# Optimization experiments

Hardware: AMD Instinct MI355X
Metric: run time of the kernel (lower is better)

The kernel has to match this reference:

```python
import jax, jax.numpy as jnp
import numpy as np

N_USER = 1_000_000
N_ITEM = 100_000
E = 16          # embedding_size
O = 16          # out_size per head
H = 4           # head_num
HID = 32        # hidden_size
B = 8192        # batch
S = 200         # sample_num
L = 50          # history length
NSUPP = 50_000  # supp_user_num


def _xavier(key, shape):
    fan_in, fan_out = shape[-2], shape[-1]
    std = np.sqrt(2.0 / (fan_in + fan_out))
    return (jax.random.normal(key, shape) * std).astype(jnp.float32)


def setup_inputs() -> dict:
    key = jax.random.key(0)
    ks = jax.random.split(key, 16)
    uid = jax.random.randint(ks[0], (B,), 0, N_USER)
    iid = jax.random.randint(ks[1], (B,), 0, N_ITEM)
    return {
        "user_embedding": _xavier(ks[2], (N_USER, E)),
        "item_embedding": _xavier(ks[3], (N_ITEM, E)),
        "wq": _xavier(ks[4], (H, E, O)),   # per-head Wq (no bias)
        "wk": _xavier(ks[5], (H, E, O)),
        "wv": _xavier(ks[6], (H, O, O)),
        "w_out": _xavier(ks[7], (H * O, O)),
        "l1_w": _xavier(ks[8], (3 * E, HID)),
        "l1_b": jnp.full((HID,), 0.1, jnp.float32),
        "l2_w": _xavier(ks[9], (HID, HID // 2)),
        "l2_b": jnp.full((HID // 2,), 0.1, jnp.float32),
        "l3_w": _xavier(ks[10], (HID // 2, 1)),
        "l3_b": jnp.full((1,), 0.1, jnp.float32),
        "user_bias": jnp.zeros((N_USER, 1), jnp.float32),
        "item_bias": jnp.zeros((N_ITEM, 1), jnp.float32),
        "x": jnp.stack([uid, iid], axis=1),                          # [B,2]
        "history": jax.random.randint(ks[11], (B, L), 0, N_ITEM),    # [B,L]
        "history_len": jax.random.randint(ks[12], (B,), 1, L + 1),   # [B] >=1
        "supp_users": jax.random.randint(ks[13], (NSUPP,), 0, N_USER),
        "sample_index": jax.random.randint(ks[14], (H, B, S), 0, NSUPP),
    }


def reference(user_embedding, item_embedding, wq, wk, wv, w_out,
              l1_w, l1_b, l2_w, l2_b, l3_w, l3_b, user_bias, item_bias,
              x, history, history_len, supp_users, sample_index):
    user_id = x[:, 0]
    item_id = x[:, 1]

    # user init embedding = mean-by-len of full (unmasked) history, as in source
    hist_emb = item_embedding[history]                                # [B,L,E]
    user_init = hist_emb.sum(axis=1) / history_len[:, None].astype(jnp.float32)  # [B,E]

    # per-head GAT over sampled support users (all heads vectorized)
    nb = user_embedding[supp_users[sample_index]]                     # [H,B,S,E]
    q = jnp.einsum('be,heo->hbo', user_init, wq)                      # [H,B,O]
    k = jnp.einsum('hbse,heo->hbso', nb, wk)                          # [H,B,S,O]
    attn = jax.nn.softmax(jnp.einsum('hbo,hbso->hbs', q, k), axis=-1)
    ctx = jnp.einsum('hbs,hbso->hbo', attn, k)                        # [H,B,O]
    gat = jnp.einsum('hbo,hop->hbp', ctx, wv)                         # [H,B,O]
    gat = jnp.transpose(gat, (1, 0, 2)).reshape(B, H * O)             # concat heads

    user_emb = gat @ w_out                                            # [B,O]
    item_emb = item_embedding[item_id]                                # [B,E]
    interaction = user_emb * item_emb
    ratings = interaction.sum(axis=1)

    h = jnp.concatenate([user_emb, item_emb, interaction], axis=1)    # [B,3E]
    x1 = jnp.tanh(h @ l1_w + l1_b)
    x2 = jnp.tanh(x1 @ l2_w + l2_b)
    x3 = (x2 @ l3_w + l3_b).reshape(-1)

    ub = user_bias[user_id, 0]
    ib = item_bias[item_id, 0]
    return (ratings + x3) / 2.0 + ub + ib
```

## Files before the change

kernel.cpp:

```cpp
#include <hip/hip_runtime.h>
#include <math.h>

#define N_USERS 1000000
#define N_ITEMS 100000
#define EMB 16
#define OUTD 16
#define NH 4
#define HID 32
#define BB 8192
#define SS 200
#define LL 50
#define NSUPP 50000

typedef float v4f __attribute__((ext_vector_type(4)));
typedef _Float16 h4 __attribute__((ext_vector_type(4)));
typedef _Float16 h2 __attribute__((ext_vector_type(2)));

__global__ __launch_bounds__(256) void prep_kernel(
    const float* __restrict__ user_emb,
    const int*   __restrict__ supp_users,
    const float* __restrict__ wk,
    _Float16*    __restrict__ Ksupp,
    const float* __restrict__ item_emb,
    const int*   __restrict__ history,
    const int*   __restrict__ history_len,
    const float* __restrict__ wq,
    float*       __restrict__ qbuf)
{
    __shared__ float s_wk[NH * EMB * OUTD];
    __shared__ float s_u[16][EMB];
    __shared__ float s_ui[4][EMB];
    __shared__ float s_wq[NH * EMB * OUTD];

    int t = threadIdx.x;
    if (blockIdx.x < NSUPP / 16) {
        for (int i = t; i < NH * EMB * OUTD; i += 256) s_wk[i] = wk[i];
        int n0 = blockIdx.x * 16;
        {
            int ul = t >> 4, e = t & 15;
            int row = supp_users[n0 + ul];
            s_u[ul][e] = user_emb[(size_t)row * EMB + e];
        }
        __syncthreads();
        int h   = t >> 6;
        int sub = (t >> 4) & 3;
        int o   = t & 15;
#pragma unroll
        for (int r = 0; r < 4; ++r) {
            int ul = sub + 4 * r;
            float acc = 0.f;
#pragma unroll
            for (int e = 0; e < EMB; ++e)
                acc += s_u[ul][e] * s_wk[(h * EMB + e) * OUTD + o];
            Ksupp[((size_t)h * NSUPP + n0 + ul) * OUTD + o] = (_Float16)acc;
        }
    } else {
        for (int i = t; i < NH * EMB * OUTD; i += 256) s_wq[i] = wq[i];
        int g    = t >> 6;
        int lane = t & 63;
        int l4   = lane >> 4;
        int e    = lane & 15;
        int b    = (blockIdx.x - NSUPP / 16) * 4 + g;

        float sum = 0.f;
        for (int l = l4; l < LL; l += 4) {
            int it = __builtin_nontemporal_load(history + (size_t)b * LL + l);
            sum += item_emb[(size_t)it * EMB + e];
        }
        sum += __shfl_xor(sum, 16);
        sum += __shfl_xor(sum, 32);
        if (lane < EMB) s_ui[g][lane] = sum / (float)history_len[b];
        __syncthreads();

        int h = (t >> 4) & 3;
        int o = t & 15;
        float acc = 0.f;
#pragma unroll
        for (int ee = 0; ee < EMB; ++ee)
            acc += s_ui[g][ee] * s_wq[(h * EMB + ee) * OUTD + o];
        qbuf[((size_t)b * NH + h) * OUTD + o] = acc;
    }
}

__global__ __launch_bounds__(256, 8) void attn_kernel(
    const _Float16* __restrict__ Ksupp,
    const float* __restrict__ qbuf,
    const int*   __restrict__ sample_index,
    const float* __restrict__ wv,
    float*       __restrict__ gat)
{
    int blk   = blockIdx.x;
    int h     = (blk & 7) >> 1;
    int btile = ((blk >> 3) << 1) | (blk & 1);
    int wave  = threadIdx.x >> 6;
    int lane  = threadIdx.x & 63;
    int b     = btile * 4 + wave;
    int g     = lane >> 2;
    int qt    = lane & 3;

    const int* si = sample_index + ((size_t)h * BB + b) * SS;
    int pre0 = __builtin_nontemporal_load(si + lane);
    int pre1 = __builtin_nontemporal_load(si + lane + 64);
    int pre2 = __builtin_nontemporal_load(si + lane + 128);
    int pre3 = (lane < 8) ? __builtin_nontemporal_load(si + lane + 192) : 0;

    v4f qv = __builtin_nontemporal_load(
        (const v4f*)(qbuf + ((size_t)b * NH + h) * OUTD) + qt);
    h4 qh = __builtin_convertvector(qv, h4);
    h2 qlo = {qh.x, qh.y};
    h2 qhi = {qh.z, qh.w};

    const h4* K4 = (const h4*)(Ksupp + (size_t)h * NSUPP * OUTD);

    int idx[13];
#pragma unroll
    for (int r = 0; r < 13; ++r) {
        int pre = (r < 4) ? pre0 : (r < 8) ? pre1 : (r < 12) ? pre2 : pre3;
        idx[r] = __shfl(pre, (r & 3) * 16 + g, 64);
    }

    h4 kq[13];
#pragma unroll
    for (int r = 0; r < 13; ++r)
        kq[r] = K4[idx[r] * 4 + qt];

    float l = 0.f;
    v4f c = {0.f, 0.f, 0.f, 0.f};
#pragma unroll
    for (int r = 0; r < 13; ++r) {
        h2 klo = {kq[r].x, kq[r].y};
        h2 khi = {kq[r].z, kq[r].w};
        float p = __builtin_amdgcn_fdot2(klo, qlo,
                  __builtin_amdgcn_fdot2(khi, qhi, 0.f, false), false);
        p += __shfl_xor(p, 1);
        p += __shfl_xor(p, 2);
        float w = __expf(p);
        if (r == 12) w = (g < 8) ? w : 0.f;
        l += w;
        v4f kf = __builtin_convertvector(kq[r], v4f);
        c += w * kf;
    }
#pragma unroll
    for (int off = 4; off < 64; off <<= 1) {
        l   += __shfl_xor(l, off);
        c.x += __shfl_xor(c.x, off);
        c.y += __shfl_xor(c.y, off);
        c.z += __shfl_xor(c.z, off);
        c.w += __shfl_xor(c.w, off);
    }
    float inv = 1.f / l;

    float part = c.x * wv[((size_t)h * OUTD + qt * 4 + 0) * OUTD + g]
               + c.y * wv[((size_t)h * OUTD + qt * 4 + 1) * OUTD + g]
               + c.z * wv[((size_t)h * OUTD + qt * 4 + 2) * OUTD + g]
               + c.w * wv[((size_t)h * OUTD + qt * 4 + 3) * OUTD + g];
    part += __shfl_xor(part, 1);
    part += __shfl_xor(part, 2);
    if (qt == 0)
        gat[(size_t)b * (NH * OUTD) + h * OUTD + g] = part * inv;
}

__global__ __launch_bounds__(256) void epilogue_kernel(
    const float* __restrict__ gat,
    const float* __restrict__ item_emb,
    const float* __restrict__ w_out,
    const float* __restrict__ l1_w, const float* __restrict__ l1_b,
    const float* __restrict__ l2_w, const float* __restrict__ l2_b,
    const float* __restrict__ l3_w, const float* __restrict__ l3_b,
    const float* __restrict__ user_bias, const float* __restrict__ item_bias,
    const int*   __restrict__ x,
    float*       __restrict__ out)
{
    int t    = threadIdx.x;
    int g    = t >> 6;
    int lane = t & 63;
    int b    = blockIdx.x * 4 + g;

    __shared__ float s_gat[4][NH * OUTD];
    __shared__ float s_ue[4][OUTD];
    __shared__ float s_ie[4][EMB];
    __shared__ float s_x1[4][HID];
    __shared__ float s_x2[4][HID / 2];

    int uid = x[(size_t)b * 2 + 0];
    int iid = x[(size_t)b * 2 + 1];

    s_gat[g][lane] = gat[(size_t)b * (NH * OUTD) + lane];
    if (lane < EMB) s_ie[g][lane] = item_emb[(size_t)iid * EMB + lane];
    __syncthreads();

    if (lane < OUTD) {
        float acc = 0.f;
#pragma unroll
        for (int j = 0; j < NH * OUTD; ++j) acc += s_gat[g][j] * w_out[j * OUTD + lane];
        s_ue[g][lane] = acc;
    }
    __syncthreads();

    if (lane < HID) {
        float acc = l1_b[lane];
#pragma unroll
        for (int i = 0; i < EMB; ++i) {
            float ue = s_ue[g][i], ie = s_ie[g][i];
            acc += ue * l1_w[i * HID + lane]
                 + ie * l1_w[(EMB + i) * HID + lane]
                 + ue * ie * l1_w[(2 * EMB + i) * HID + lane];
        }
        s_x1[g][lane] = tanhf(acc);
    }
    __syncthreads();

    if (lane < HID / 2) {
        float acc = l2_b[lane];
#pragma unroll
        for (int j = 0; j < HID; ++j) acc += s_x1[g][j] * l2_w[j * (HID / 2) + lane];
        s_x2[g][lane] = tanhf(acc);
    }
    __syncthreads();

    if (lane == 0) {
        float x3 = l3_b[0];
#pragma unroll
        for (int j = 0; j < HID / 2; ++j) x3 += s_x2[g][j] * l3_w[j];
        float ratings = 0.f;
#pragma unroll
        for (int o = 0; o < OUTD; ++o) ratings += s_ue[g][o] * s_ie[g][o];
        out[b] = 0.5f * (ratings + x3) + user_bias[uid] + item_bias[iid];
    }
}

extern "C" void kernel_launch(void* const* d_in, const int* in_sizes, int n_in,
                              void* d_out, int out_size, void* d_ws, size_t ws_size,
                              hipStream_t stream) {
    const float* user_embedding = (const float*)d_in[0];
    const float* item_embedding = (const float*)d_in[1];
    const float* wq             = (const float*)d_in[2];
    const float* wk             = (const float*)d_in[3];
    const float* wv             = (const float*)d_in[4];
    const float* w_out          = (const float*)d_in[5];
    const float* l1_w           = (const float*)d_in[6];
    const float* l1_b           = (const float*)d_in[7];
    const float* l2_w           = (const float*)d_in[8];
    const float* l2_b           = (const float*)d_in[9];
    const float* l3_w           = (const float*)d_in[10];
    const float* l3_b           = (const float*)d_in[11];
    const float* user_bias      = (const float*)d_in[12];
    const float* item_bias      = (const float*)d_in[13];
    const int*   x              = (const int*)d_in[14];
    const int*   history        = (const int*)d_in[15];
    const int*   history_len    = (const int*)d_in[16];
    const int*   supp_users     = (const int*)d_in[17];
    const int*   sample_index   = (const int*)d_in[18];
    float* out = (float*)d_out;

    char* ws = (char*)d_ws;
    _Float16* Ksupp = (_Float16*)ws;
    ws += (size_t)NH * NSUPP * OUTD * sizeof(_Float16);
    float* qbuf  = (float*)ws;
    ws += (size_t)BB * NH * OUTD * sizeof(float);
    float* gat   = (float*)ws;

    prep_kernel<<<NSUPP / 16 + BB / 4, 256, 0, stream>>>(
        user_embedding, supp_users, wk, Ksupp,
        item_embedding, history, history_len, wq, qbuf);
    attn_kernel<<<NH * BB / 4, 256, 0, stream>>>(Ksupp, qbuf, sample_index, wv, gat);
    epilogue_kernel<<<BB / 4, 256, 0, stream>>>(
        gat, item_embedding, w_out, l1_w, l1_b, l2_w, l2_b, l3_w, l3_b,
        user_bias, item_bias, x, out);
}
```

Baseline: 220.1 us.

## Fold Wk into query and Wv, gather raw fp16 support embeddings, fuse epilogue

Reassociates the attention maths. The query is pre-multiplied by Wk^T, so scores come straight from raw support-user embeddings. Wk·Wv is precomputed so the context projection uses a single combined matrix. The per-head K table (4x50000x16) becomes one shared fp16 embedding table of 50000x16, which cuts table build work and the footprint of the gathers. The attention and epilogue kernels are merged, each block handling 4 batch rows across 4 head-waves, which removes the gat round-trip and one launch but lowers the launch bound to 4 and serializes 4 rows per wave.

Result: faster. 201.2 us (median of 2 runs) (-8.6%).

```diff
diff --git a/kernel.cpp b/kernel.cpp
--- a/kernel.cpp
+++ b/kernel.cpp
@@ -13,49 +13,42 @@
 #define NSUPP 50000
 
 typedef float v4f __attribute__((ext_vector_type(4)));
+typedef _Float16 h2 __attribute__((ext_vector_type(2)));
 typedef _Float16 h4 __attribute__((ext_vector_type(4)));
-typedef _Float16 h2 __attribute__((ext_vector_type(2)));
+
+#define WAVE_SYNC() do { asm volatile("s_waitcnt lgkmcnt(0)" ::: "memory"); \
+                         __builtin_amdgcn_sched_barrier(0); } while (0)
 
 __global__ __launch_bounds__(256) void prep_kernel(
     const float* __restrict__ user_emb,
     const int*   __restrict__ supp_users,
     const float* __restrict__ wk,
-    _Float16*    __restrict__ Ksupp,
+    const float* __restrict__ wq,
+    const float* __restrict__ wv,
     const float* __restrict__ item_emb,
     const int*   __restrict__ history,
     const int*   __restrict__ history_len,
-    const float* __restrict__ wq,
-    float*       __restrict__ qbuf)
+    _Float16*    __restrict__ tbl,
+    _Float16*    __restrict__ qtbuf,
+    float*       __restrict__ Wkv)
 {
-    __shared__ float s_wk[NH * EMB * OUTD];
-    __shared__ float s_u[16][EMB];
     __shared__ float s_ui[4][EMB];
     __shared__ float s_wq[NH * EMB * OUTD];
+    __shared__ float s_wk[NH * EMB * OUTD];
+    __shared__ float s_q[4][NH * OUTD];
 
     int t = threadIdx.x;
     if (blockIdx.x < NSUPP / 16) {
-        for (int i = t; i < NH * EMB * OUTD; i += 256) s_wk[i] = wk[i];
         int n0 = blockIdx.x * 16;
-        {
-            int ul = t >> 4, e = t & 15;
-            int row = supp_users[n0 + ul];
-            s_u[ul][e] = user_emb[(size_t)row * EMB + e];
-        }
-        __syncthreads();
-        int h   = t >> 6;
-        int sub = (t >> 4) & 3;
-        int o   = t & 15;
-#pragma unroll
-        for (int r = 0; r < 4; ++r) {
-            int ul = sub + 4 * r;
-            float acc = 0.f;
-#pragma unroll
-            for (int e = 0; e < EMB; ++e)
-                acc += s_u[ul][e] * s_wk[(h * EMB + e) * OUTD + o];
-            Ksupp[((size_t)h * NSUPP + n0 + ul) * OUTD + o] = (_Float16)acc;
-        }
-    } else {
-        for (int i = t; i < NH * EMB * OUTD; i += 256) s_wq[i] = wq[i];
+        int ul = t >> 4, e = t & 15;
+        int row = supp_users[n0 + ul];
+        tbl[(size_t)(n0 + ul) * EMB + e] =
+            (_Float16)user_emb[(size_t)row * EMB + e];
+    } else if (blockIdx.x < NSUPP / 16 + BB / 4) {
+        for (int i = t; i < NH * EMB * OUTD; i += 256) {
+            s_wq[i] = wq[i];
+            s_wk[i] = wk[i];
+        }
         int g    = t >> 6;
         int lane = t & 63;
         int l4   = lane >> 4;
@@ -78,90 +71,31 @@
 #pragma unroll
         for (int ee = 0; ee < EMB; ++ee)
             acc += s_ui[g][ee] * s_wq[(h * EMB + ee) * OUTD + o];
-        qbuf[((size_t)b * NH + h) * OUTD + o] = acc;
+        s_q[g][h * OUTD + o] = acc;
+        __syncthreads();
+
+        float qt = 0.f;
+#pragma unroll
+        for (int oo = 0; oo < OUTD; ++oo)
+            qt += s_wk[(h * EMB + o) * OUTD + oo] * s_q[g][h * OUTD + oo];
+        qtbuf[((size_t)b * NH + h) * EMB + o] = (_Float16)qt;
+    } else {
+        for (int i = t; i < NH * EMB * OUTD; i += 256) {
+            int h = i >> 8, e = (i >> 4) & 15, p = i & 15;
+            float a = 0.f;
+#pragma unroll
+            for (int o = 0; o < OUTD; ++o)
+                a += wk[(h * EMB + e) * OUTD + o] * wv[(h * OUTD + o) * OUTD + p];
+            Wkv[i] = a;
+        }
     }
 }
 
-__global__ __launch_bounds__(256, 8) void attn_kernel(
-    const _Float16* __restrict__ Ksupp,
-    const float* __restrict__ qbuf,
+__global__ __launch_bounds__(256, 4) void attn_epi_kernel(
+    const _Float16* __restrict__ tbl,
+    const _Float16* __restrict__ qtbuf,
     const int*   __restrict__ sample_index,
-    const float* __restrict__ wv,
-    float*       __restrict__ gat)
-{
-    int blk   = blockIdx.x;
-    int h     = (blk & 7) >> 1;
-    int btile = ((blk >> 3) << 1) | (blk & 1);
-    int wave  = threadIdx.x >> 6;
-    int lane  = threadIdx.x & 63;
-    int b     = btile * 4 + wave;
-    int g     = lane >> 2;
-    int qt    = lane & 3;
-
-    const int* si = sample_index + ((size_t)h * BB + b) * SS;
-    int pre0 = __builtin_nontemporal_load(si + lane);
-    int pre1 = __builtin_nontemporal_load(si + lane + 64);
-    int pre2 = __builtin_nontemporal_load(si + lane + 128);
-    int pre3 = (lane < 8) ? __builtin_nontemporal_load(si + lane + 192) : 0;
-
-    v4f qv = __builtin_nontemporal_load(
-        (const v4f*)(qbuf + ((size_t)b * NH + h) * OUTD) + qt);
-    h4 qh = __builtin_convertvector(qv, h4);
-    h2 qlo = {qh.x, qh.y};
-    h2 qhi = {qh.z, qh.w};
-
-    const h4* K4 = (const h4*)(Ksupp + (size_t)h * NSUPP * OUTD);
-
-    int idx[13];
-#pragma unroll
-    for (int r = 0; r < 13; ++r) {
-        int pre = (r < 4) ? pre0 : (r < 8) ? pre1 : (r < 12) ? pre2 : pre3;
-        idx[r] = __shfl(pre, (r & 3) * 16 + g, 64);
-    }
-
-    h4 kq[13];
-#pragma unroll
-    for (int r = 0; r < 13; ++r)
-        kq[r] = K4[idx[r] * 4 + qt];
-
-    float l = 0.f;
-    v4f c = {0.f, 0.f, 0.f, 0.f};
-#pragma unroll
-    for (int r = 0; r < 13; ++r) {
-        h2 klo = {kq[r].x, kq[r].y};
-        h2 khi = {kq[r].z, kq[r].w};
-        float p = __builtin_amdgcn_fdot2(klo, qlo,
-                  __builtin_amdgcn_fdot2(khi, qhi, 0.f, false), false);
-        p += __shfl_xor(p, 1);
-        p += __shfl_xor(p, 2);
-        float w = __expf(p);
-        if (r == 12) w = (g < 8) ? w : 0.f;
-        l += w;
-        v4f kf = __builtin_convertvector(kq[r], v4f);
-        c += w * kf;
-    }
-#pragma unroll
-    for (int off = 4; off < 64; off <<= 1) {
-        l   += __shfl_xor(l, off);
-        c.x += __shfl_xor(c.x, off);
-        c.y += __shfl_xor(c.y, off);
-        c.z += __shfl_xor(c.z, off);
-        c.w += __shfl_xor(c.w, off);
-    }
-    float inv = 1.f / l;
-
-    float part = c.x * wv[((size_t)h * OUTD + qt * 4 + 0) * OUTD + g]
-               + c.y * wv[((size_t)h * OUTD + qt * 4 + 1) * OUTD + g]
-               + c.z * wv[((size_t)h * OUTD + qt * 4 + 2) * OUTD + g]
-               + c.w * wv[((size_t)h * OUTD + qt * 4 + 3) * OUTD + g];
-    part += __shfl_xor(part, 1);
-    part += __shfl_xor(part, 2);
-    if (qt == 0)
-        gat[(size_t)b * (NH * OUTD) + h * OUTD + g] = part * inv;
-}
-
-__global__ __launch_bounds__(256) void epilogue_kernel(
-    const float* __restrict__ gat,
+    const float* __restrict__ Wkv,
     const float* __restrict__ item_emb,
     const float* __restrict__ w_out,
     const float* __restrict__ l1_w, const float* __restrict__ l1_b,
@@ -171,60 +105,123 @@
     const int*   __restrict__ x,
     float*       __restrict__ out)
 {
-    int t    = threadIdx.x;
-    int g    = t >> 6;
-    int lane = t & 63;
-    int b    = blockIdx.x * 4 + g;
-
     __shared__ float s_gat[4][NH * OUTD];
     __shared__ float s_ue[4][OUTD];
     __shared__ float s_ie[4][EMB];
     __shared__ float s_x1[4][HID];
     __shared__ float s_x2[4][HID / 2];
 
+    int h    = threadIdx.x >> 6;
+    int lane = threadIdx.x & 63;
+    int g    = lane >> 2;
+    int qt   = lane & 3;
+
+    const h4* U4 = (const h4*)tbl;
+
+    for (int bl = 0; bl < 4; ++bl) {
+        int b = blockIdx.x * 4 + bl;
+
+        const int* si = sample_index + ((size_t)h * BB + b) * SS;
+        int pre0 = __builtin_nontemporal_load(si + lane);
+        int pre1 = __builtin_nontemporal_load(si + lane + 64);
+        int pre2 = __builtin_nontemporal_load(si + lane + 128);
+        int pre3 = (lane < 8) ? __builtin_nontemporal_load(si + lane + 192) : 0;
+
+        h4 qh = ((const h4*)(qtbuf + ((size_t)b * NH + h) * EMB))[qt];
+        h2 qlo = {qh.x, qh.y};
+        h2 qhi = {qh.z, qh.w};
+
+        int idx[13];
+#pragma unroll
+        for (int r = 0; r < 13; ++r) {
+            int pre = (r < 4) ? pre0 : (r < 8) ? pre1 : (r < 12) ? pre2 : pre3;
+            idx[r] = __shfl(pre, (r & 3) * 16 + g, 64);
+        }
+
+        h4 kq[13];
+#pragma unroll
+        for (int r = 0; r < 13; ++r)
+            kq[r] = U4[(size_t)idx[r] * 4 + qt];
+
+        float l = 0.f;
+        v4f c = {0.f, 0.f, 0.f, 0.f};
+#pragma unroll
+        for (int r = 0; r < 13; ++r) {
+            h2 klo = {kq[r].x, kq[r].y};
+            h2 khi = {kq[r].z, kq[r].w};
+            float p = __builtin_amdgcn_fdot2(klo, qlo,
+                      __builtin_amdgcn_fdot2(khi, qhi, 0.f, false), false);
+            p += __shfl_xor(p, 1);
+            p += __shfl_xor(p, 2);
+            float w = __expf(p);
+            if (r == 12) w = (g < 8) ? w : 0.f;
+            l += w;
+            c += w * __builtin_convertvector(kq[r], v4f);
+        }
+#pragma unroll
+        for (int off = 4; off < 64; off <<= 1) {
+            l   += __shfl_xor(l, off);
+            c.x += __shfl_xor(c.x, off);
+            c.y += __shfl_xor(c.y, off);
+            c.z += __shfl_xor(c.z, off);
+            c.w += __shfl_xor(c.w, off);
+        }
+        float inv = 1.f / l;
+
+        float part = c.x * Wkv[((size_t)h * EMB + qt * 4 + 0) * OUTD + g]
+                   + c.y * Wkv[((size_t)h * EMB + qt * 4 + 1) * OUTD + g]
+                   + c.z * Wkv[((size_t)h * EMB + qt * 4 + 2) * OUTD + g]
+                   + c.w * Wkv[((size_t)h * EMB + qt * 4 + 3) * OUTD + g];
+        part += __shfl_xor(part, 1);
+        part += __shfl_xor(part, 2);
+        if (qt == 0)
+            s_gat[bl][h * OUTD + g] = part * inv;
+    }
+    __syncthreads();
+
+    int b   = blockIdx.x * 4 + h;
     int uid = x[(size_t)b * 2 + 0];
     int iid = x[(size_t)b * 2 + 1];
 
-    s_gat[g][lane] = gat[(size_t)b * (NH * OUTD) + lane];
-    if (lane < EMB) s_ie[g][lane] = item_emb[(size_t)iid * EMB + lane];
-    __syncthreads();
-
+    if (lane < EMB) s_ie[h][lane] = item_emb[(size_t)iid * EMB + lane];
     if (lane < OUTD) {
         float acc = 0.f;
 #pragma unroll
-        for (int j = 0; j < NH * OUTD; ++j) acc += s_gat[g][j] * w_out[j * OUTD + lane];
-        s_ue[g][lane] = acc;
-    }
-    __syncthreads();
+        for (int j = 0; j < NH * OUTD; ++j)
+            acc += s_gat[h][j] * w_out[j * OUTD + lane];
+        s_ue[h][lane] = acc;
+    }
+    WAVE_SYNC();
 
     if (lane < HID) {
         float acc = l1_b[lane];
 #pragma unroll
         for (int i = 0; i < EMB; ++i) {
-            float ue = s_ue[g][i], ie = s_ie[g][i];
+            float ue = s_ue[h][i], ie = s_ie[h][i];
             acc += ue * l1_w[i * HID + lane]
                  + ie * l1_w[(EMB + i) * HID + lane]
                  + ue * ie * l1_w[(2 * EMB + i) * HID + lane];
         }
-        s_x1[g][lane] = tanhf(acc);
-    }
-    __syncthreads();
+        s_x1[h][lane] = tanhf(acc);
+    }
+    WAVE_SYNC();
 
     if (lane < HID / 2) {
         float acc = l2_b[lane];
 #pragma unroll
-        for (int j = 0; j < HID; ++j) acc += s_x1[g][j] * l2_w[j * (HID / 2) + lane];
-        s_x2[g][lane] = tanhf(acc);
-    }
-    __syncthreads();
+        for (int j = 0; j < HID; ++j)
+            acc += s_x1[h][j] * l2_w[j * (HID / 2) + lane];
+        s_x2[h][lane] = tanhf(acc);
+    }
+    WAVE_SYNC();
 
     if (lane == 0) {
         float x3 = l3_b[0];
 #pragma unroll
-        for (int j = 0; j < HID / 2; ++j) x3 += s_x2[g][j] * l3_w[j];
+        for (int j = 0; j < HID / 2; ++j) x3 += s_x2[h][j] * l3_w[j];
         float ratings = 0.f;
 #pragma unroll
-        for (int o = 0; o < OUTD; ++o) ratings += s_ue[g][o] * s_ie[g][o];
+        for (int o = 0; o < OUTD; ++o) ratings += s_ue[h][o] * s_ie[h][o];
         out[b] = 0.5f * (ratings + x3) + user_bias[uid] + item_bias[iid];
     }
 }
@@ -254,17 +251,17 @@
     float* out = (float*)d_out;
 
     char* ws = (char*)d_ws;
-    _Float16* Ksupp = (_Float16*)ws;
-    ws += (size_t)NH * NSUPP * OUTD * sizeof(_Float16);
-    float* qbuf  = (float*)ws;
-    ws += (size_t)BB * NH * OUTD * sizeof(float);
-    float* gat   = (float*)ws;
-
-    prep_kernel<<<NSUPP / 16 + BB / 4, 256, 0, stream>>>(
-        user_embedding, supp_users, wk, Ksupp,
-        item_embedding, history, history_len, wq, qbuf);
-    attn_kernel<<<NH * BB / 4, 256, 0, stream>>>(Ksupp, qbuf, sample_index, wv, gat);
-    epilogue_kernel<<<BB / 4, 256, 0, stream>>>(
-        gat, item_embedding, w_out, l1_w, l1_b, l2_w, l2_b, l3_w, l3_b,
+    _Float16* tbl = (_Float16*)ws;
+    ws += (size_t)NSUPP * EMB * sizeof(_Float16);
+    _Float16* qtbuf = (_Float16*)ws;
+    ws += (size_t)BB * NH * EMB * sizeof(_Float16);
+    float* Wkv = (float*)ws;
+
+    prep_kernel<<<NSUPP / 16 + BB / 4 + 1, 256, 0, stream>>>(
+        user_embedding, supp_users, wk, wq, wv,
+        item_embedding, history, history_len, tbl, qtbuf, Wkv);
+    attn_epi_kernel<<<BB / 4, 256, 0, stream>>>(
+        tbl, qtbuf, sample_index, Wkv, item_embedding, w_out,
+        l1_w, l1_b, l2_w, l2_b, l3_w, l3_b,
         user_bias, item_bias, x, out);
 }
```
